# Optimization experiments

Hardware: AMD Instinct MI355X
Metric: run time of the kernel (lower is better)

Reference implementation:

```python
import jax, jax.numpy as jnp
import numpy as np

KH = KW = 3
STRIDE = 1
PAD = 1
DIL = 1


def im2col(x, kh, kw, stride, pad, dil):
    """F.unfold equivalent: x (N,C,H,W) -> (N,C,kh,kw,oh,ow)."""
    n, c, h, w = x.shape
    oh = (h + 2 * pad - dil * (kh - 1) - 1) // stride + 1
    ow = (w + 2 * pad - dil * (kw - 1) - 1) // stride + 1
    xp = jnp.pad(x, ((0, 0), (0, 0), (pad, pad), (pad, pad)))
    rows = []
    for i in range(kh):
        cols = []
        for j in range(kw):
            patch = jax.lax.slice(
                xp,
                (0, 0, i * dil, j * dil),
                (n, c, i * dil + (oh - 1) * stride + 1, j * dil + (ow - 1) * stride + 1),
                (1, 1, stride, stride),
            )  # (N,C,oh,ow)
            cols.append(patch)
        rows.append(jnp.stack(cols, axis=2))  # (N,C,kw,oh,ow)
    return jnp.stack(rows, axis=2)  # (N,C,kh,kw,oh,ow)


def setup_inputs() -> dict:
    key = jax.random.key(0)
    k1, k2, k3, k4 = jax.random.split(key, 4)
    N, Cin, Cout, H, W = 4, 64, 64, 128, 128
    x = jax.random.normal(k1, (N, Cin, H, W), dtype=jnp.float32)
    # adapting kernel: positive values (softmax-like output in EdgeKernel2d)
    kernel = jax.random.uniform(k2, (N, 1, KH, KW, H, W), dtype=jnp.float32, minval=0.01, maxval=1.0)
    fan_in = Cin * KH * KW
    weight = jax.random.normal(k3, (Cout, Cin, KH, KW), dtype=jnp.float32) * (1.0 / np.sqrt(fan_in))
    bias = jax.random.normal(k4, (Cout,), dtype=jnp.float32) * 0.01
    return {"x": x, "kernel": kernel, "weight": weight, "bias": bias}


def reference(x, kernel, weight, bias):
    # im_cols: (N,Cin,kh,kw,oh,ow)
    im_cols = im2col(x, KH, KW, STRIDE, PAD, DIL)
    in_mul_k = im_cols * kernel  # kernel broadcasts over Cin
    # dominate = sum_{k,l} in_mul_k / sum_{k,l} kernel  -> (N,Cin,oh,ow)
    dominate = in_mul_k.sum(axis=(2, 3)) / kernel.sum(axis=(2, 3))
    corrected = in_mul_k + dominate[:, :, None, None] * (1.0 - kernel)
    out = jnp.einsum('ncklhw,ockl->nohw', corrected, weight)
    out = out + bias[None, :, None, None]
    return out
```

## Files before the change

kernel.cpp:

```cpp
#include <hip/hip_runtime.h>
#include <hip/hip_bf16.h>
#include <cstddef>

typedef __attribute__((ext_vector_type(8))) short bf16x8;
typedef __attribute__((ext_vector_type(4))) float f32x4;
typedef __attribute__((ext_vector_type(2))) unsigned int u32x2;

#define NB 4
#define CIN 64
#define COUT 64
#define HH 128
#define WW 128
#define TAPS 9
#define PX 64
#define KCH 160
#define KTOT 640
#define STRD 82

__device__ __forceinline__ unsigned short f2bf(float f) {
    union { float f; unsigned u; } v; v.f = f;
    unsigned u = v.u + 0x7FFFu + ((v.u >> 16) & 1u);
    return (unsigned short)(u >> 16);
}

__global__ void prep_weight(const float* __restrict__ w, unsigned short* __restrict__ wB,
                            float* __restrict__ zrow) {
    int idx = blockIdx.x * blockDim.x + threadIdx.x;
    if (idx < 68) zrow[idx] = 0.f;
    if (idx >= COUT * KTOT) return;
    int o = idx / KTOT;
    int kk = idx - o * KTOT;
    int chunk = kk / KCH;
    int kl = kk - chunk * KCH;
    unsigned short v = 0;
    if (kl < 16 * TAPS) {
        int tap = kl >> 4;
        int cl = kl & 15;
        v = f2bf(w[(o * CIN + chunk * 16 + cl) * TAPS + tap]);
    }
    wB[idx] = v;
}

__launch_bounds__(256, 4)
__global__ void pac_conv(const float* __restrict__ x, const float* __restrict__ Kp,
                         const unsigned short* __restrict__ wB,
                         const float* __restrict__ bias,
                         const float* __restrict__ zrow1,
                         float* __restrict__ out) {
    __shared__ unsigned int sCor[PX][STRD];

    const int blk = blockIdx.x;
    const int w0 = (blk & 1) * PX;
    const int h  = (blk >> 1) & (HH - 1);
    const int n  = blk >> 8;
    const int t    = threadIdx.x;
    const int lane = t & 63;
    const int wv   = __builtin_amdgcn_readfirstlane(t >> 6);

    float kreg[TAPS];
    float ks = 0.f;
    const float* kp = Kp + ((size_t)n * TAPS * HH + h) * WW + w0 + lane;
    #pragma unroll
    for (int tap = 0; tap < TAPS; ++tap) {
        kreg[tap] = kp[(size_t)tap * HH * WW];
        ks += kreg[tap];
    }
    const float inv = 1.0f / ks;

    for (int i = t; i < PX * 8; i += 256) sCor[i >> 3][72 + (i & 7)] = 0u;

    const bool mL = (w0 == 0) && (lane == 0);
    const bool mR = (w0 != 0) && (lane == 63);
    const unsigned voffL = (mL ? 1u : (unsigned)lane) * 4u;
    const unsigned voffC = ((unsigned)lane + 1u) * 4u;
    const unsigned voffR = (mR ? 64u : (unsigned)lane + 2u) * 4u;

    const int l15 = lane & 15;
    const int kg  = (lane >> 4) * 8;
    const float bval = bias[wv * 16 + l15];

    f32x4 acc[4];
    #pragma unroll
    for (int i = 0; i < 4; ++i) acc[i] = (f32x4){0.f, 0.f, 0.f, 0.f};

    for (int chunk = 0; chunk < 4; ++chunk) {
        const int c0 = chunk * 16 + wv * 4;
        const float* xb = x + (size_t)(n * CIN + c0) * (HH * WW) + w0 - 1;

        float xv[4][TAPS];
        #pragma unroll
        for (int k = 0; k < 3; ++k) {
            const int hh = h + k - 1;
            const bool hok = (unsigned)hh < (unsigned)HH;
            #pragma unroll
            for (int j = 0; j < 4; ++j) {
                const float* p = hok ? (xb + (size_t)j * (HH * WW) + hh * WW) : (zrow1 - 1);
                float vL = *(const float*)((const char*)p + voffL);
                float vC = *(const float*)((const char*)p + voffC);
                float vR = *(const float*)((const char*)p + voffR);
                xv[j][k * 3 + 0] = mL ? 0.f : vL;
                xv[j][k * 3 + 1] = vC;
                xv[j][k * 3 + 2] = mR ? 0.f : vR;
            }
        }

        u32x2 cor[TAPS];
        float dom[4];
        #pragma unroll
        for (int j = 0; j < 4; ++j) {
            float s = 0.f;
            #pragma unroll
            for (int tap = 0; tap < TAPS; ++tap) s = fmaf(xv[j][tap], kreg[tap], s);
            dom[j] = s * inv;
        }
        #pragma unroll
        for (int tap = 0; tap < TAPS; ++tap) {
            float c01[4];
            #pragma unroll
            for (int j = 0; j < 4; ++j)
                c01[j] = fmaf(kreg[tap], xv[j][tap] - dom[j], dom[j]);
            union { __hip_bfloat162 h2; unsigned int u; } a, b;
            a.h2 = __float22bfloat162_rn(make_float2(c01[0], c01[1]));
            b.h2 = __float22bfloat162_rn(make_float2(c01[2], c01[3]));
            cor[tap] = (u32x2){a.u, b.u};
        }

        if (chunk) __syncthreads();
        #pragma unroll
        for (int tap = 0; tap < TAPS; ++tap)
            *reinterpret_cast<u32x2*>(&sCor[lane][tap * 8 + wv * 2]) = cor[tap];
        __syncthreads();

        const unsigned short* wrow = wB + (size_t)(wv * 16 + l15) * KTOT + chunk * KCH + kg;
        #pragma unroll
        for (int step = 0; step < 5; ++step) {
            bf16x8 bfrag = *reinterpret_cast<const bf16x8*>(wrow + step * 32);
            #pragma unroll
            for (int pt = 0; pt < 4; ++pt) {
                const unsigned int* ap = &sCor[pt * 16 + l15][(step * 32 + kg) >> 1];
                u32x2 alo = *reinterpret_cast<const u32x2*>(ap);
                u32x2 ahi = *reinterpret_cast<const u32x2*>(ap + 2);
                union { u32x2 p[2]; bf16x8 f; } af;
                af.p[0] = alo; af.p[1] = ahi;
                acc[pt] = __builtin_amdgcn_mfma_f32_16x16x32_bf16(af.f, bfrag, acc[pt], 0, 0, 0);
            }
        }
    }

    const int o = wv * 16 + l15;
    const int pxq = (lane >> 4) * 4;
    float* op = out + (((size_t)n * COUT + o) * HH + h) * WW + w0 + pxq;
    #pragma unroll
    for (int pt = 0; pt < 4; ++pt) {
        f32x4 v = acc[pt];
        #pragma unroll
        for (int r = 0; r < 4; ++r) v[r] += bval;
        *reinterpret_cast<f32x4*>(op + pt * 16) = v;
    }
}

extern "C" void kernel_launch(void* const* d_in, const int* in_sizes, int n_in,
                              void* d_out, int out_size, void* d_ws, size_t ws_size,
                              hipStream_t stream) {
    const float* x    = (const float*)d_in[0];
    const float* Kp   = (const float*)d_in[1];
    const float* wgt  = (const float*)d_in[2];
    const float* bias = (const float*)d_in[3];
    float* out = (float*)d_out;
    unsigned short* wB = (unsigned short*)d_ws;
    float* zrow = (float*)((char*)d_ws + 81920);

    prep_weight<<<(COUT * KTOT + 255) / 256, 256, 0, stream>>>(wgt, wB, zrow);

    pac_conv<<<NB * HH * (WW / PX), 256, 0, stream>>>(x, Kp, wB, bias, zrow + 1, out);
}
```

Measured before the change: 30.65 us.

## Process full rows per block, use DPP lane shifts for horizontal taps

Each block now covers a whole 128-pixel output row with 512 threads (two 64-pixel halves) in place of two 64-pixel blocks of 256 threads. Left and right neighbor values come from DPP row shifts of the centre load, so each row needs one global load plus a halo load on a single lane, replacing the three loads per row. The LDS A-fragment read becomes one 128-bit load with a padded stride, and the block index is swizzled. This cuts redundant global loads and LDS instructions, at the cost of lower occupancy bounds and extra DPP and branch work.

```diff
diff --git a/kernel.cpp b/kernel.cpp
--- a/kernel.cpp
+++ b/kernel.cpp
@@ -5,6 +5,7 @@
 typedef __attribute__((ext_vector_type(8))) short bf16x8;
 typedef __attribute__((ext_vector_type(4))) float f32x4;
 typedef __attribute__((ext_vector_type(2))) unsigned int u32x2;
+typedef __attribute__((ext_vector_type(4))) unsigned int u32x4;
 
 #define NB 4
 #define CIN 64
@@ -12,10 +13,18 @@
 #define HH 128
 #define WW 128
 #define TAPS 9
-#define PX 64
 #define KCH 160
 #define KTOT 640
-#define STRD 82
+#define STRD 84
+
+__device__ __forceinline__ float dpp_shr1(float v) {
+    int r = __builtin_amdgcn_update_dpp(0, __builtin_bit_cast(int, v), 0x138, 0xF, 0xF, true);
+    return __builtin_bit_cast(float, r);
+}
+__device__ __forceinline__ float dpp_shl1(float v) {
+    int r = __builtin_amdgcn_update_dpp(0, __builtin_bit_cast(int, v), 0x130, 0xF, 0xF, true);
+    return __builtin_bit_cast(float, r);
+}
 
 __device__ __forceinline__ unsigned short f2bf(float f) {
     union { float f; unsigned u; } v; v.f = f;
@@ -26,7 +35,7 @@
 __global__ void prep_weight(const float* __restrict__ w, unsigned short* __restrict__ wB,
                             float* __restrict__ zrow) {
     int idx = blockIdx.x * blockDim.x + threadIdx.x;
-    if (idx < 68) zrow[idx] = 0.f;
+    if (idx < 192) zrow[idx] = 0.f;
     if (idx >= COUT * KTOT) return;
     int o = idx / KTOT;
     int kk = idx - o * KTOT;
@@ -41,25 +50,29 @@
     wB[idx] = v;
 }
 
-__launch_bounds__(256, 4)
+__launch_bounds__(512)
 __global__ void pac_conv(const float* __restrict__ x, const float* __restrict__ Kp,
                          const unsigned short* __restrict__ wB,
                          const float* __restrict__ bias,
-                         const float* __restrict__ zrow1,
+                         const float* __restrict__ zrow,
                          float* __restrict__ out) {
-    __shared__ unsigned int sCor[PX][STRD];
+    __shared__ __align__(16) unsigned int sCor[128][STRD];
 
-    const int blk = blockIdx.x;
-    const int w0 = (blk & 1) * PX;
-    const int h  = (blk >> 1) & (HH - 1);
-    const int n  = blk >> 8;
-    const int t    = threadIdx.x;
+    const int blk0 = blockIdx.x;
+    const int blk  = ((blk0 & 7) << 6) | (blk0 >> 3);
+    const int h = blk & (HH - 1);
+    const int n = blk >> 7;
+
+    const int t = threadIdx.x;
     const int lane = t & 63;
-    const int wv   = __builtin_amdgcn_readfirstlane(t >> 6);
+    const int w = __builtin_amdgcn_readfirstlane(t >> 6);
+    const int q = w & 3;
+    const int half = w >> 2;
+    const int px = half * 64 + lane;
 
+    const float* kp = Kp + (size_t)n * TAPS * HH * WW + (size_t)h * WW + px;
     float kreg[TAPS];
     float ks = 0.f;
-    const float* kp = Kp + ((size_t)n * TAPS * HH + h) * WW + w0 + lane;
     #pragma unroll
     for (int tap = 0; tap < TAPS; ++tap) {
         kreg[tap] = kp[(size_t)tap * HH * WW];
@@ -67,89 +80,83 @@
     }
     const float inv = 1.0f / ks;
 
-    for (int i = t; i < PX * 8; i += 256) sCor[i >> 3][72 + (i & 7)] = 0u;
+    for (int i = t; i < 128 * 8; i += 512) sCor[i >> 3][72 + (i & 7)] = 0u;
 
-    const bool mL = (w0 == 0) && (lane == 0);
-    const bool mR = (w0 != 0) && (lane == 63);
-    const unsigned voffL = (mL ? 1u : (unsigned)lane) * 4u;
-    const unsigned voffC = ((unsigned)lane + 1u) * 4u;
-    const unsigned voffR = (mR ? 64u : (unsigned)lane + 2u) * 4u;
+    const bool hneed = (half == 0) ? (lane == 63) : (lane == 0);
+    const int  hoff  = (half == 0) ? 64 : 63;
 
     const int l15 = lane & 15;
-    const int kg  = (lane >> 4) * 8;
-    const float bval = bias[wv * 16 + l15];
+    const int g   = lane >> 4;
 
     f32x4 acc[4];
     #pragma unroll
     for (int i = 0; i < 4; ++i) acc[i] = (f32x4){0.f, 0.f, 0.f, 0.f};
 
     for (int chunk = 0; chunk < 4; ++chunk) {
-        const int c0 = chunk * 16 + wv * 4;
-        const float* xb = x + (size_t)(n * CIN + c0) * (HH * WW) + w0 - 1;
-
-        float xv[4][TAPS];
-        #pragma unroll
-        for (int k = 0; k < 3; ++k) {
-            const int hh = h + k - 1;
-            const bool hok = (unsigned)hh < (unsigned)HH;
-            #pragma unroll
-            for (int j = 0; j < 4; ++j) {
-                const float* p = hok ? (xb + (size_t)j * (HH * WW) + hh * WW) : (zrow1 - 1);
-                float vL = *(const float*)((const char*)p + voffL);
-                float vC = *(const float*)((const char*)p + voffC);
-                float vR = *(const float*)((const char*)p + voffR);
-                xv[j][k * 3 + 0] = mL ? 0.f : vL;
-                xv[j][k * 3 + 1] = vC;
-                xv[j][k * 3 + 2] = mR ? 0.f : vR;
-            }
-        }
-
         u32x2 cor[TAPS];
-        float dom[4];
+        float prev[TAPS];
         #pragma unroll
         for (int j = 0; j < 4; ++j) {
+            const int c = chunk * 16 + q * 4 + j;
+            const float* xrow0 = x + ((size_t)(n * CIN + c) * HH) * WW;
+            float xv[TAPS];
+            #pragma unroll
+            for (int k = 0; k < 3; ++k) {
+                const int hh = h + k - 1;
+                const float* rp = ((unsigned)hh < (unsigned)HH) ? (xrow0 + (size_t)hh * WW) : zrow;
+                const float vC = rp[px];
+                float hv = 0.f;
+                if (hneed) hv = rp[hoff];
+                float vL = dpp_shr1(vC);
+                float vR = dpp_shl1(vC);
+                if (half == 0) { if (lane == 63) vR = hv; }
+                else           { if (lane == 0)  vL = hv; }
+                xv[k * 3 + 0] = vL;
+                xv[k * 3 + 1] = vC;
+                xv[k * 3 + 2] = vR;
+            }
             float s = 0.f;
             #pragma unroll
-            for (int tap = 0; tap < TAPS; ++tap) s = fmaf(xv[j][tap], kreg[tap], s);
-            dom[j] = s * inv;
-        }
-        #pragma unroll
-        for (int tap = 0; tap < TAPS; ++tap) {
-            float c01[4];
-            #pragma unroll
-            for (int j = 0; j < 4; ++j)
-                c01[j] = fmaf(kreg[tap], xv[j][tap] - dom[j], dom[j]);
-            union { __hip_bfloat162 h2; unsigned int u; } a, b;
-            a.h2 = __float22bfloat162_rn(make_float2(c01[0], c01[1]));
-            b.h2 = __float22bfloat162_rn(make_float2(c01[2], c01[3]));
-            cor[tap] = (u32x2){a.u, b.u};
+            for (int tap = 0; tap < TAPS; ++tap) s = fmaf(xv[tap], kreg[tap], s);
+            const float d = s * inv;
+            if (j & 1) {
+                #pragma unroll
+                for (int tap = 0; tap < TAPS; ++tap) {
+                    float cc = fmaf(kreg[tap], xv[tap] - d, d);
+                    union { __hip_bfloat162 h2; unsigned int u; } pk;
+                    pk.h2 = __float22bfloat162_rn(make_float2(prev[tap], cc));
+                    cor[tap][j >> 1] = pk.u;
+                }
+            } else {
+                #pragma unroll
+                for (int tap = 0; tap < TAPS; ++tap)
+                    prev[tap] = fmaf(kreg[tap], xv[tap] - d, d);
+            }
         }
 
         if (chunk) __syncthreads();
         #pragma unroll
         for (int tap = 0; tap < TAPS; ++tap)
-            *reinterpret_cast<u32x2*>(&sCor[lane][tap * 8 + wv * 2]) = cor[tap];
+            *reinterpret_cast<u32x2*>(&sCor[px][tap * 8 + q * 2]) = cor[tap];
         __syncthreads();
 
-        const unsigned short* wrow = wB + (size_t)(wv * 16 + l15) * KTOT + chunk * KCH + kg;
+        const unsigned short* wrow = wB + (size_t)(q * 16 + l15) * KTOT + chunk * KCH + g * 8;
         #pragma unroll
         for (int step = 0; step < 5; ++step) {
             bf16x8 bfrag = *reinterpret_cast<const bf16x8*>(wrow + step * 32);
             #pragma unroll
             for (int pt = 0; pt < 4; ++pt) {
-                const unsigned int* ap = &sCor[pt * 16 + l15][(step * 32 + kg) >> 1];
-                u32x2 alo = *reinterpret_cast<const u32x2*>(ap);
-                u32x2 ahi = *reinterpret_cast<const u32x2*>(ap + 2);
-                union { u32x2 p[2]; bf16x8 f; } af;
-                af.p[0] = alo; af.p[1] = ahi;
-                acc[pt] = __builtin_amdgcn_mfma_f32_16x16x32_bf16(af.f, bfrag, acc[pt], 0, 0, 0);
+                const int row = half * 64 + pt * 16 + l15;
+                u32x4 a = *reinterpret_cast<const u32x4*>(&sCor[row][step * 16 + g * 4]);
+                acc[pt] = __builtin_amdgcn_mfma_f32_16x16x32_bf16(
+                    __builtin_bit_cast(bf16x8, a), bfrag, acc[pt], 0, 0, 0);
             }
         }
     }
 
-    const int o = wv * 16 + l15;
-    const int pxq = (lane >> 4) * 4;
-    float* op = out + (((size_t)n * COUT + o) * HH + h) * WW + w0 + pxq;
+    const int o = q * 16 + l15;
+    const float bval = bias[o];
+    float* op = out + (((size_t)n * COUT + o) * HH + h) * WW + half * 64 + g * 4;
     #pragma unroll
     for (int pt = 0; pt < 4; ++pt) {
         f32x4 v = acc[pt];
@@ -172,5 +179,5 @@
 
     prep_weight<<<(COUT * KTOT + 255) / 256, 256, 0, stream>>>(wgt, wB, zrow);
 
-    pac_conv<<<NB * HH * (WW / PX), 256, 0, stream>>>(x, Kp, wB, bias, zrow + 1, out);
+    pac_conv<<<NB * HH, 512, 0, stream>>>(x, Kp, wB, bias, zrow, out);
 }
```

Result: slower. 35.09 us (+14.5%).

## Double-buffer LDS corrected tiles and drop K padding with a masked tail MFMA

Applied to the files above, without the earlier changes.

The shared corrected-patch buffer is split into two buffers. The MFMA work for the previous channel chunk now runs after the next chunk's global loads and bf16 packing are issued, and one barrier per chunk replaces two. The K dimension per chunk shrinks from 160 padded to 144 exact. This removes the zero-padded weight columns and the LDS zero fill, and the last 16 K values are handled by a half-masked MFMA. The per-channel computation is also reordered to lower register pressure, at the cost of twice the LDS footprint.

```diff
diff --git a/kernel.cpp b/kernel.cpp
--- a/kernel.cpp
+++ b/kernel.cpp
@@ -5,6 +5,7 @@
 typedef __attribute__((ext_vector_type(8))) short bf16x8;
 typedef __attribute__((ext_vector_type(4))) float f32x4;
 typedef __attribute__((ext_vector_type(2))) unsigned int u32x2;
+typedef __attribute__((ext_vector_type(4))) unsigned int u32x4;
 
 #define NB 4
 #define CIN 64
@@ -12,10 +13,10 @@
 #define HH 128
 #define WW 128
 #define TAPS 9
-#define PX 64
-#define KCH 160
-#define KTOT 640
-#define STRD 82
+#define KCH 144
+#define KTOT 576
+#define STRD 76
+#define BUFD (64 * STRD)
 
 __device__ __forceinline__ unsigned short f2bf(float f) {
     union { float f; unsigned u; } v; v.f = f;
@@ -26,19 +27,15 @@
 __global__ void prep_weight(const float* __restrict__ w, unsigned short* __restrict__ wB,
                             float* __restrict__ zrow) {
     int idx = blockIdx.x * blockDim.x + threadIdx.x;
-    if (idx < 68) zrow[idx] = 0.f;
+    if (idx < 192) zrow[idx] = 0.f;
     if (idx >= COUT * KTOT) return;
     int o = idx / KTOT;
     int kk = idx - o * KTOT;
     int chunk = kk / KCH;
     int kl = kk - chunk * KCH;
-    unsigned short v = 0;
-    if (kl < 16 * TAPS) {
-        int tap = kl >> 4;
-        int cl = kl & 15;
-        v = f2bf(w[(o * CIN + chunk * 16 + cl) * TAPS + tap]);
-    }
-    wB[idx] = v;
+    int tap = kl >> 4;
+    int cl = kl & 15;
+    wB[idx] = f2bf(w[(o * CIN + chunk * 16 + cl) * TAPS + tap]);
 }
 
 __launch_bounds__(256, 4)
@@ -47,10 +44,10 @@
                          const float* __restrict__ bias,
                          const float* __restrict__ zrow1,
                          float* __restrict__ out) {
-    __shared__ unsigned int sCor[PX][STRD];
+    __shared__ __align__(16) unsigned int sCor[2][BUFD];
 
     const int blk = blockIdx.x;
-    const int w0 = (blk & 1) * PX;
+    const int w0 = (blk & 1) * 64;
     const int h  = (blk >> 1) & (HH - 1);
     const int n  = blk >> 8;
     const int t    = threadIdx.x;
@@ -67,8 +64,6 @@
     }
     const float inv = 1.0f / ks;
 
-    for (int i = t; i < PX * 8; i += 256) sCor[i >> 3][72 + (i & 7)] = 0u;
-
     const bool mL = (w0 == 0) && (lane == 0);
     const bool mR = (w0 != 0) && (lane == 63);
     const unsigned voffL = (mL ? 1u : (unsigned)lane) * 4u;
@@ -76,80 +71,99 @@
     const unsigned voffR = (mR ? 64u : (unsigned)lane + 2u) * 4u;
 
     const int l15 = lane & 15;
-    const int kg  = (lane >> 4) * 8;
+    const int g   = lane >> 4;
+    const int gg  = g & 1;
+    const bool gok = (g < 2);
     const float bval = bias[wv * 16 + l15];
 
     f32x4 acc[4];
     #pragma unroll
     for (int i = 0; i < 4; ++i) acc[i] = (f32x4){0.f, 0.f, 0.f, 0.f};
 
+    auto mfma_chunk = [&](int c) {
+        const unsigned int* src = &sCor[c & 1][0];
+        const unsigned short* wrow = wB + (size_t)(wv * 16 + l15) * KTOT + c * KCH + g * 8;
+        #pragma unroll
+        for (int step = 0; step < 4; ++step) {
+            bf16x8 bfrag = *reinterpret_cast<const bf16x8*>(wrow + step * 32);
+            #pragma unroll
+            for (int pt = 0; pt < 4; ++pt) {
+                u32x4 a = *reinterpret_cast<const u32x4*>(
+                    &src[(pt * 16 + l15) * STRD + step * 16 + g * 4]);
+                acc[pt] = __builtin_amdgcn_mfma_f32_16x16x32_bf16(
+                    __builtin_bit_cast(bf16x8, a), bfrag, acc[pt], 0, 0, 0);
+            }
+        }
+        const unsigned short* wtail =
+            wB + (size_t)(wv * 16 + l15) * KTOT + c * KCH + 128 + gg * 8;
+        u32x4 bu = *reinterpret_cast<const u32x4*>(wtail);
+        if (!gok) bu = (u32x4){0u, 0u, 0u, 0u};
+        bf16x8 btail = __builtin_bit_cast(bf16x8, bu);
+        #pragma unroll
+        for (int pt = 0; pt < 4; ++pt) {
+            u32x4 a = *reinterpret_cast<const u32x4*>(
+                &src[(pt * 16 + l15) * STRD + 64 + gg * 4]);
+            if (!gok) a = (u32x4){0u, 0u, 0u, 0u};
+            acc[pt] = __builtin_amdgcn_mfma_f32_16x16x32_bf16(
+                __builtin_bit_cast(bf16x8, a), btail, acc[pt], 0, 0, 0);
+        }
+    };
+
+    #pragma unroll
     for (int chunk = 0; chunk < 4; ++chunk) {
-        const int c0 = chunk * 16 + wv * 4;
-        const float* xb = x + (size_t)(n * CIN + c0) * (HH * WW) + w0 - 1;
-
-        float xv[4][TAPS];
-        #pragma unroll
-        for (int k = 0; k < 3; ++k) {
-            const int hh = h + k - 1;
-            const bool hok = (unsigned)hh < (unsigned)HH;
+        u32x2 cor[TAPS];
+        {
+            const int c0 = chunk * 16 + wv * 4;
+            const float* xb = x + (size_t)(n * CIN + c0) * (HH * WW) + w0 - 1;
+            float prev[TAPS];
             #pragma unroll
             for (int j = 0; j < 4; ++j) {
-                const float* p = hok ? (xb + (size_t)j * (HH * WW) + hh * WW) : (zrow1 - 1);
-                float vL = *(const float*)((const char*)p + voffL);
-                float vC = *(const float*)((const char*)p + voffC);
-                float vR = *(const float*)((const char*)p + voffR);
-                xv[j][k * 3 + 0] = mL ? 0.f : vL;
-                xv[j][k * 3 + 1] = vC;
-                xv[j][k * 3 + 2] = mR ? 0.f : vR;
+                float xv[TAPS];
+                #pragma unroll
+                for (int k = 0; k < 3; ++k) {
+                    const int hh2 = h + k - 1;
+                    const float* p = ((unsigned)hh2 < (unsigned)HH)
+                        ? (xb + (size_t)j * (HH * WW) + (size_t)hh2 * WW)
+                        : (zrow1 - 1);
+                    float vL = *(const float*)((const char*)p + voffL);
+                    float vC = *(const float*)((const char*)p + voffC);
+                    float vR = *(const float*)((const char*)p + voffR);
+                    xv[k * 3 + 0] = mL ? 0.f : vL;
+                    xv[k * 3 + 1] = vC;
+                    xv[k * 3 + 2] = mR ? 0.f : vR;
+                }
+                float s = 0.f;
+                #pragma unroll
+                for (int tap = 0; tap < TAPS; ++tap) s = fmaf(xv[tap], kreg[tap], s);
+                const float d = s * inv;
+                if (j & 1) {
+                    #pragma unroll
+                    for (int tap = 0; tap < TAPS; ++tap) {
+                        float cc = fmaf(kreg[tap], xv[tap] - d, d);
+                        union { __hip_bfloat162 h2; unsigned int u; } pk;
+                        pk.h2 = __float22bfloat162_rn(make_float2(prev[tap], cc));
+                        cor[tap][j >> 1] = pk.u;
+                    }
+                } else {
+                    #pragma unroll
+                    for (int tap = 0; tap < TAPS; ++tap)
+                        prev[tap] = fmaf(kreg[tap], xv[tap] - d, d);
+                }
             }
         }
 
-        u32x2 cor[TAPS];
-        float dom[4];
-        #pragma unroll
-        for (int j = 0; j < 4; ++j) {
-            float s = 0.f;
-            #pragma unroll
-            for (int tap = 0; tap < TAPS; ++tap) s = fmaf(xv[j][tap], kreg[tap], s);
-            dom[j] = s * inv;
-        }
-        #pragma unroll
-        for (int tap = 0; tap < TAPS; ++tap) {
-            float c01[4];
-            #pragma unroll
-            for (int j = 0; j < 4; ++j)
-                c01[j] = fmaf(kreg[tap], xv[j][tap] - dom[j], dom[j]);
-            union { __hip_bfloat162 h2; unsigned int u; } a, b;
-            a.h2 = __float22bfloat162_rn(make_float2(c01[0], c01[1]));
-            b.h2 = __float22bfloat162_rn(make_float2(c01[2], c01[3]));
-            cor[tap] = (u32x2){a.u, b.u};
-        }
+        if (chunk > 0) mfma_chunk(chunk - 1);
 
-        if (chunk) __syncthreads();
+        unsigned int* dst = &sCor[chunk & 1][lane * STRD + wv * 2];
         #pragma unroll
         for (int tap = 0; tap < TAPS; ++tap)
-            *reinterpret_cast<u32x2*>(&sCor[lane][tap * 8 + wv * 2]) = cor[tap];
+            *reinterpret_cast<u32x2*>(dst + tap * 8) = cor[tap];
         __syncthreads();
-
-        const unsigned short* wrow = wB + (size_t)(wv * 16 + l15) * KTOT + chunk * KCH + kg;
-        #pragma unroll
-        for (int step = 0; step < 5; ++step) {
-            bf16x8 bfrag = *reinterpret_cast<const bf16x8*>(wrow + step * 32);
-            #pragma unroll
-            for (int pt = 0; pt < 4; ++pt) {
-                const unsigned int* ap = &sCor[pt * 16 + l15][(step * 32 + kg) >> 1];
-                u32x2 alo = *reinterpret_cast<const u32x2*>(ap);
-                u32x2 ahi = *reinterpret_cast<const u32x2*>(ap + 2);
-                union { u32x2 p[2]; bf16x8 f; } af;
-                af.p[0] = alo; af.p[1] = ahi;
-                acc[pt] = __builtin_amdgcn_mfma_f32_16x16x32_bf16(af.f, bfrag, acc[pt], 0, 0, 0);
-            }
-        }
     }
+    mfma_chunk(3);
 
     const int o = wv * 16 + l15;
-    const int pxq = (lane >> 4) * 4;
-    float* op = out + (((size_t)n * COUT + o) * HH + h) * WW + w0 + pxq;
+    float* op = out + (((size_t)n * COUT + o) * HH + h) * WW + w0 + g * 4;
     #pragma unroll
     for (int pt = 0; pt < 4; ++pt) {
         f32x4 v = acc[pt];
@@ -168,9 +182,9 @@
     const float* bias = (const float*)d_in[3];
     float* out = (float*)d_out;
     unsigned short* wB = (unsigned short*)d_ws;
-    float* zrow = (float*)((char*)d_ws + 81920);
+    float* zrow = (float*)((char*)d_ws + 73728);
 
     prep_weight<<<(COUT * KTOT + 255) / 256, 256, 0, stream>>>(wgt, wB, zrow);
 
-    pac_conv<<<NB * HH * (WW / PX), 256, 0, stream>>>(x, Kp, wB, bias, zrow + 1, out);
+    pac_conv<<<NB * HH * 2, 256, 0, stream>>>(x, Kp, wB, bias, zrow + 1, out);
 }
```

Result: slower. 40.91 us (+33.4%).
